# Kernel optimization log

Measured on AMD Instinct MI355X. Metric: run time of the kernel, lower is better.

## Reference

```python
import jax, jax.numpy as jnp
import numpy as np

VOCAB_SIZE = 95
EMBED_DIM = 48
HIDDEN_DIM = 48


def setup_inputs() -> dict:
    key = jax.random.key(0)
    ks = jax.random.split(key, 8)
    B, S = 2048, 512
    x = jax.random.randint(ks[0], (B, S), 0, VOCAB_SIZE)
    s_e = 1.0  # torch Embedding default init ~ N(0,1); scale irrelevant for correctness
    emb = jax.random.normal(ks[1], (VOCAB_SIZE, EMBED_DIM), dtype=jnp.float32) * s_e
    k = 1.0 / np.sqrt(HIDDEN_DIM)
    w_ih = jax.random.uniform(ks[2], (3 * HIDDEN_DIM, EMBED_DIM), minval=-k, maxval=k, dtype=jnp.float32)
    w_hh = jax.random.uniform(ks[3], (3 * HIDDEN_DIM, HIDDEN_DIM), minval=-k, maxval=k, dtype=jnp.float32)
    b_ih = jax.random.uniform(ks[4], (3 * HIDDEN_DIM,), minval=-k, maxval=k, dtype=jnp.float32)
    b_hh = jax.random.uniform(ks[5], (3 * HIDDEN_DIM,), minval=-k, maxval=k, dtype=jnp.float32)
    w_out = jax.random.uniform(ks[6], (VOCAB_SIZE, HIDDEN_DIM), minval=-k, maxval=k, dtype=jnp.float32)
    b_out = jax.random.uniform(ks[7], (VOCAB_SIZE,), minval=-k, maxval=k, dtype=jnp.float32)
    return {"x": x, "emb": emb, "w_ih": w_ih, "w_hh": w_hh,
            "b_ih": b_ih, "b_hh": b_hh, "w_out": w_out, "b_out": b_out}


def _gru(embed, w_ih, w_hh, b_ih, b_hh):
    # embed: [B, S, E]. PyTorch GRU (single layer, batch_first):
    #   r = sig(Wir x + bir + Whr h + bhr); z = sig(Wiz x + biz + Whz h + bhz)
    B = embed.shape[0]
    H = w_hh.shape[1]
    # precompute input contributions for all timesteps: [S, B, 3H]
    xg = jnp.einsum('bse,ge->bsg', embed, w_ih) + b_ih
    xg = jnp.swapaxes(xg, 0, 1)
    h0 = jnp.zeros((B, H), dtype=embed.dtype)

    def step(h, xg_t):
        gh = h @ w_hh.T + b_hh  # [B, 3H]
        xr, xz, xn = jnp.split(xg_t, 3, axis=-1)
        hr, hz, hn = jnp.split(gh, 3, axis=-1)
        r = jax.nn.sigmoid(xr + hr)
        z = jax.nn.sigmoid(xz + hz)
        n = jnp.tanh(xn + r * hn)
        h_new = (1.0 - z) * n + z * h
        return h_new, h_new

    h_last, hs = jax.lax.scan(step, h0, xg)
    out = jnp.swapaxes(hs, 0, 1)  # [B, S, H]
    return out, h_last


def reference(x, emb, w_ih, w_hh, b_ih, b_hh, w_out, b_out):
    embed = emb[x]  # [B, S, E]
    out, h_last = _gru(embed, w_ih, w_hh, b_ih, b_hh)
    logits = jnp.einsum('bsh,vh->bsv', out, w_out) + b_out  # [B, S, V]
    hidden = h_last[None]  # [1, B, H] to match torch GRU hidden layout
    return logits, hidden
```

## Files before the change

kernel.cpp:

```cpp
#include <hip/hip_runtime.h>
#include <hip/hip_bf16.h>


#define BATCH 2048
#define SEQ   512
#define HDIM  48
#define VOCAB 95
#define G3    144
#define LPOS  64

__device__ __forceinline__ float sigmoidf_(float x) {
    return 1.0f / (1.0f + __expf(-x));
}

__global__ void xg_precompute(const float* __restrict__ emb,
                              const float* __restrict__ w_ih,
                              const float* __restrict__ b_ih,
                              float* __restrict__ xg) {
    int v = blockIdx.x;
    int g = threadIdx.x;
    const float* e = emb + v * HDIM;
    const float* w = w_ih + g * HDIM;
    float a0 = 0.f, a1 = 0.f, a2 = 0.f, a3 = 0.f;
    #pragma unroll
    for (int k = 0; k < HDIM; k += 4) {
        a0 = fmaf(w[k + 0], e[k + 0], a0);
        a1 = fmaf(w[k + 1], e[k + 1], a1);
        a2 = fmaf(w[k + 2], e[k + 2], a2);
        a3 = fmaf(w[k + 3], e[k + 3], a3);
    }
    xg[v * G3 + g] = b_ih[g] + ((a0 + a1) + (a2 + a3));
}

__global__ __launch_bounds__(64, 2)
void gru_rec(const int* __restrict__ x,
             const float* __restrict__ xg_table,
             const float* __restrict__ w_hh,
             const float* __restrict__ b_hh,
             float* __restrict__ out,
             float* __restrict__ hidden) {
    const int row = blockIdx.x;
    const int j   = threadIdx.x;
    __shared__ float hsh[HDIM];

    float4 wr[12], wz[12], wn[12];
    float br = 0.f, bz = 0.f, bn = 0.f;
    float hj = 0.f;
    if (j < HDIM) {
        const float4* whr = (const float4*)(w_hh + (j         ) * HDIM);
        const float4* whz = (const float4*)(w_hh + (j +   HDIM) * HDIM);
        const float4* whn = (const float4*)(w_hh + (j + 2*HDIM) * HDIM);
        #pragma unroll
        for (int k = 0; k < 12; ++k) { wr[k] = whr[k]; wz[k] = whz[k]; wn[k] = whn[k]; }
        br = b_hh[j]; bz = b_hh[j + HDIM]; bn = b_hh[j + 2*HDIM];
        hsh[j] = 0.f;
    }
    __syncthreads();

    const int* xrow = x + row * SEQ;
    int tok = xrow[0];
    for (int t = 0; t < SEQ; ++t) {
        int tok_next = (t + 1 < SEQ) ? xrow[t + 1] : 0;
        float hnew = 0.f;
        if (j < HDIM) {
            const float* xg = xg_table + tok * G3;
            float xr = xg[j], xz = xg[j + HDIM], xn = xg[j + 2*HDIM];
            float accr = br, accz = bz, accn = bn;
            const float4* h4 = (const float4*)hsh;
            #pragma unroll
            for (int k = 0; k < 12; ++k) {
                float4 hh = h4[k];
                accr = fmaf(wr[k].x, hh.x, accr); accr = fmaf(wr[k].y, hh.y, accr);
                accr = fmaf(wr[k].z, hh.z, accr); accr = fmaf(wr[k].w, hh.w, accr);
                accz = fmaf(wz[k].x, hh.x, accz); accz = fmaf(wz[k].y, hh.y, accz);
                accz = fmaf(wz[k].z, hh.z, accz); accz = fmaf(wz[k].w, hh.w, accz);
                accn = fmaf(wn[k].x, hh.x, accn); accn = fmaf(wn[k].y, hh.y, accn);
                accn = fmaf(wn[k].z, hh.z, accn); accn = fmaf(wn[k].w, hh.w, accn);
            }
            float r = sigmoidf_(xr + accr);
            float z = sigmoidf_(xz + accz);
            float n = tanhf(xn + r * accn);
            hnew = (1.0f - z) * n + z * hj;
            hj = hnew;
            out[((long)(row * SEQ + t)) * VOCAB + j] = hnew;
        }
        __syncthreads();
        if (j < HDIM) hsh[j] = hnew;
        __syncthreads();
        tok = tok_next;
    }
    if (j < HDIM) hidden[row * HDIM + j] = hj;
}

__global__ __launch_bounds__(256, 4)
void logits_k(const float* __restrict__ w_out,
              const float* __restrict__ b_out,
              float* __restrict__ out) {
    __shared__ __align__(16) float lsm[LPOS * VOCAB];

    const long pos0 = (long)blockIdx.x * LPOS;
    const int  tid  = threadIdx.x;
    const int  lane = tid & 63;
    const int  wv   = __builtin_amdgcn_readfirstlane(tid >> 6);

    for (int i = tid; i < LPOS * HDIM; i += 256) {
        int p = i / HDIM;
        int k = i - p * HDIM;
        lsm[p * 49 + k] = out[(pos0 + p) * VOCAB + k];
    }
    __syncthreads();

    const int p = lane;
    float h[HDIM];
    #pragma unroll
    for (int k = 0; k < HDIM; ++k) h[k] = lsm[p * 49 + k];
    __syncthreads();

    const int v0 = wv * 24;
    const int v1 = (v0 + 24 < VOCAB) ? (v0 + 24) : VOCAB;
    for (int v = v0; v < v1; ++v) {
        const float* w = w_out + v * HDIM;
        float a0 = 0.f, a1 = 0.f, a2 = 0.f, a3 = 0.f;
        #pragma unroll
        for (int k = 0; k < HDIM; k += 4) {
            a0 = fmaf(w[k + 0], h[k + 0], a0);
            a1 = fmaf(w[k + 1], h[k + 1], a1);
            a2 = fmaf(w[k + 2], h[k + 2], a2);
            a3 = fmaf(w[k + 3], h[k + 3], a3);
        }
        lsm[p * VOCAB + v] = b_out[v] + ((a0 + a1) + (a2 + a3));
    }
    __syncthreads();

    float4*       dst = (float4*)(out + pos0 * VOCAB);
    const float4* src = (const float4*)lsm;
    for (int i = tid; i < (LPOS * VOCAB) / 4; i += 256)
        dst[i] = src[i];
}

extern "C" void kernel_launch(void* const* d_in, const int* in_sizes, int n_in,
                              void* d_out, int out_size, void* d_ws, size_t ws_size,
                              hipStream_t stream) {
    const int*   x     = (const int*)d_in[0];
    const float* emb   = (const float*)d_in[1];
    const float* w_ih  = (const float*)d_in[2];
    const float* w_hh  = (const float*)d_in[3];
    const float* b_ih  = (const float*)d_in[4];
    const float* b_hh  = (const float*)d_in[5];
    const float* w_out = (const float*)d_in[6];
    const float* b_out = (const float*)d_in[7];

    float* out    = (float*)d_out;
    float* hidden = out + (long)BATCH * SEQ * VOCAB;
    float* xg     = (float*)d_ws;

    xg_precompute<<<VOCAB, G3, 0, stream>>>(emb, w_ih, b_ih, xg);
    gru_rec<<<BATCH, 64, 0, stream>>>(x, xg, w_hh, b_hh, out, hidden);
    logits_k<<<(BATCH * SEQ) / LPOS, 256, 0, stream>>>(w_out, b_out, out);
}
```

Baseline: 1.166 ms.

## Drop per-step barriers, prefetch next gate inputs, and stash hidden states compactly

The recurrence kernel runs as a single 64-thread wavefront, so the two per-timestep __syncthreads are removed and the shared hidden vector is updated in place. The next token's input-gate values are loaded one step ahead to hide the table-lookup latency. tanhf is replaced with an exp-based formula. Hidden states go to a dense 48-wide stash in workspace when it is large enough, which the logits kernel then reads. Dropping the barriers relies on wavefront lockstep ordering of LDS reads before writes, and the fast tanh may lose precision for large inputs.

```diff
diff --git a/kernel.cpp b/kernel.cpp
--- a/kernel.cpp
+++ b/kernel.cpp
@@ -11,6 +11,9 @@
 
 __device__ __forceinline__ float sigmoidf_(float x) {
     return 1.0f / (1.0f + __expf(-x));
+}
+__device__ __forceinline__ float tanhf_(float x) {
+    return 1.0f - 2.0f / (__expf(2.0f * x) + 1.0f);
 }
 
 __global__ void xg_precompute(const float* __restrict__ emb,
@@ -37,7 +40,8 @@
              const float* __restrict__ xg_table,
              const float* __restrict__ w_hh,
              const float* __restrict__ b_hh,
-             float* __restrict__ out,
+             float* __restrict__ stash,
+             long sstride,
              float* __restrict__ hidden) {
     const int row = blockIdx.x;
     const int j   = threadIdx.x;
@@ -59,12 +63,21 @@
 
     const int* xrow = x + row * SEQ;
     int tok = xrow[0];
+    float xr = 0.f, xz = 0.f, xn = 0.f;
+    if (j < HDIM) {
+        const float* xg0 = xg_table + tok * G3;
+        xr = xg0[j]; xz = xg0[j + HDIM]; xn = xg0[j + 2*HDIM];
+    }
+    float* srow = stash + (long)row * SEQ * sstride + j;
+
     for (int t = 0; t < SEQ; ++t) {
         int tok_next = (t + 1 < SEQ) ? xrow[t + 1] : 0;
-        float hnew = 0.f;
+        float xrn = 0.f, xzn = 0.f, xnn = 0.f;
         if (j < HDIM) {
-            const float* xg = xg_table + tok * G3;
-            float xr = xg[j], xz = xg[j + HDIM], xn = xg[j + 2*HDIM];
+            const float* xgn = xg_table + tok_next * G3;
+            xrn = xgn[j]; xzn = xgn[j + HDIM]; xnn = xgn[j + 2*HDIM];
+        }
+        if (j < HDIM) {
             float accr = br, accz = bz, accn = bn;
             const float4* h4 = (const float4*)hsh;
             #pragma unroll
@@ -79,15 +92,13 @@
             }
             float r = sigmoidf_(xr + accr);
             float z = sigmoidf_(xz + accz);
-            float n = tanhf(xn + r * accn);
-            hnew = (1.0f - z) * n + z * hj;
+            float n = tanhf_(xn + r * accn);
+            float hnew = (1.0f - z) * n + z * hj;
             hj = hnew;
-            out[((long)(row * SEQ + t)) * VOCAB + j] = hnew;
+            srow[(long)t * sstride] = hnew;
+            hsh[j] = hnew;
         }
-        __syncthreads();
-        if (j < HDIM) hsh[j] = hnew;
-        __syncthreads();
-        tok = tok_next;
+        xr = xrn; xz = xzn; xn = xnn;
     }
     if (j < HDIM) hidden[row * HDIM + j] = hj;
 }
@@ -95,6 +106,8 @@
 __global__ __launch_bounds__(256, 4)
 void logits_k(const float* __restrict__ w_out,
               const float* __restrict__ b_out,
+              const float* __restrict__ stash,
+              long sstride,
               float* __restrict__ out) {
     __shared__ __align__(16) float lsm[LPOS * VOCAB];
 
@@ -106,7 +119,7 @@
     for (int i = tid; i < LPOS * HDIM; i += 256) {
         int p = i / HDIM;
         int k = i - p * HDIM;
-        lsm[p * 49 + k] = out[(pos0 + p) * VOCAB + k];
+        lsm[p * 49 + k] = stash[(pos0 + p) * sstride + k];
     }
     __syncthreads();
 
@@ -154,7 +167,19 @@
     float* hidden = out + (long)BATCH * SEQ * VOCAB;
     float* xg     = (float*)d_ws;
 
+    size_t xg_bytes = (((size_t)VOCAB * G3 * sizeof(float)) + 255) & ~(size_t)255;
+    size_t stash_need = (size_t)BATCH * SEQ * HDIM * sizeof(float);
+    float* stash;
+    long   sstride;
+    if (ws_size >= xg_bytes + stash_need) {
+        stash   = (float*)((char*)d_ws + xg_bytes);
+        sstride = HDIM;
+    } else {
+        stash   = out;
+        sstride = VOCAB;
+    }
+
     xg_precompute<<<VOCAB, G3, 0, stream>>>(emb, w_ih, b_ih, xg);
-    gru_rec<<<BATCH, 64, 0, stream>>>(x, xg, w_hh, b_hh, out, hidden);
-    logits_k<<<(BATCH * SEQ) / LPOS, 256, 0, stream>>>(w_out, b_out, out);
+    gru_rec<<<BATCH, 64, 0, stream>>>(x, xg, w_hh, b_hh, stash, sstride, hidden);
+    logits_k<<<(BATCH * SEQ) / LPOS, 256, 0, stream>>>(w_out, b_out, stash, sstride, out);
 }
```

Result: no change. 1.163 ms (-0.3%).
